# Optimization experiments

Hardware: AMD Instinct MI355X
Metric: run time of the kernel (lower is better)

## Reference

```python
import jax, jax.numpy as jnp
import numpy as np

N_NODES = 50000
N_EDGES = 800000
OBS_DIM = 25
HID = 128
EMB = 64
EDGE_DIM = 8
HEADS = 4
N_LAYERS = 3
COMM_RANGE = 1500.0
LN_EPS = 1e-5


def layernorm(x, g, b):
    mu = jnp.mean(x, axis=-1, keepdims=True)
    var = jnp.mean((x - mu) ** 2, axis=-1, keepdims=True)
    return (x - mu) / jnp.sqrt(var + LN_EPS) * g + b


def setup_inputs() -> dict:
    key = jax.random.key(0)
    ks = iter(jax.random.split(key, 64))

    def w(shape, s=0.05):
        return (jax.random.normal(next(ks), shape, jnp.float32) * s).astype(jnp.float32)

    inp = {}
    inp["observations"] = jax.random.normal(next(ks), (N_NODES, OBS_DIM), jnp.float32)
    inp["positions"] = jax.random.uniform(next(ks), (N_NODES, 2), jnp.float32) * 1000.0
    inp["edge_index"] = jax.random.randint(next(ks), (2, N_EDGES), 0, N_NODES, jnp.int32)
    # node encoder (obs_encoder branch: Linear-LN-ReLU-Linear-ReLU)
    inp["enc_w1"] = w((OBS_DIM, HID)); inp["enc_b1"] = w((HID,), 0.01)
    inp["enc_ln_g"] = jnp.ones((HID,), jnp.float32); inp["enc_ln_b"] = jnp.zeros((HID,), jnp.float32)
    inp["enc_w2"] = w((HID, EMB)); inp["enc_b2"] = w((EMB,), 0.01)
    cat_dim = 2 * EMB + EDGE_DIM  # 136
    # per-layer GNN params, stacked over layers
    inp["msg_w1"] = w((N_LAYERS, cat_dim, HID)); inp["msg_b1"] = w((N_LAYERS, HID), 0.01)
    inp["msg_w2"] = w((N_LAYERS, HID, EMB)); inp["msg_b2"] = w((N_LAYERS, EMB), 0.01)
    inp["att_w1"] = w((N_LAYERS, cat_dim, HID)); inp["att_b1"] = w((N_LAYERS, HID), 0.01)
    inp["att_w2"] = w((N_LAYERS, HID, HEADS)); inp["att_b2"] = w((N_LAYERS, HEADS), 0.01)
    inp["upd_w1"] = w((N_LAYERS, 2 * EMB, HID)); inp["upd_b1"] = w((N_LAYERS, HID), 0.01)
    inp["upd_w2"] = w((N_LAYERS, HID, EMB)); inp["upd_b2"] = w((N_LAYERS, EMB), 0.01)
    inp["ln_g"] = jnp.ones((N_LAYERS, EMB), jnp.float32); inp["ln_b"] = jnp.zeros((N_LAYERS, EMB), jnp.float32)
    # output projection
    inp["out_w1"] = w((EMB, HID)); inp["out_b1"] = w((HID,), 0.01)
    inp["out_w2"] = w((HID, EMB)); inp["out_b2"] = w((EMB,), 0.01)
    return inp


def reference(observations, positions, edge_index,
              enc_w1, enc_b1, enc_ln_g, enc_ln_b, enc_w2, enc_b2,
              msg_w1, msg_b1, msg_w2, msg_b2,
              att_w1, att_b1, att_w2, att_b2,
              upd_w1, upd_b1, upd_w2, upd_b2,
              ln_g, ln_b,
              out_w1, out_b1, out_w2, out_b2):
    n = observations.shape[0]
    # --- node encoder (use_full_obs=True path) ---
    h = observations @ enc_w1 + enc_b1
    h = jax.nn.relu(layernorm(h, enc_ln_g, enc_ln_b))
    x = jax.nn.relu(h @ enc_w2 + enc_b2)  # [N, EMB]

    # --- edge features (build_graph math, edges given) ---
    src, dst = edge_index[0], edge_index[1]
    rel = positions[dst] - positions[src]                    # [E, 2]
    dist = jnp.linalg.norm(rel, axis=-1, keepdims=True)      # [E, 1]
    rel_n = rel / (dist + 1e-6)
    dist_n = dist / COMM_RANGE
    angle = jnp.arctan2(rel[:, 1], rel[:, 0])[:, None]
    edge_attr = jnp.concatenate(
        [dist_n, rel_n, jnp.cos(angle), jnp.sin(angle), dist_n ** 2,
         jnp.zeros((rel.shape[0], 2), x.dtype)], axis=-1)    # [E, 8]

    # --- GNN communication layers (PyG: x_i = target = dst, x_j = source = src,
    #     aggregate to dst; dropout inactive at inference) ---
    for l in range(N_LAYERS):
        cat = jnp.concatenate([x[dst], x[src], edge_attr], axis=-1)       # [E, 136]
        m = jax.nn.relu(cat @ msg_w1[l] + msg_b1[l]) @ msg_w2[l] + msg_b2[l]   # [E, EMB]
        a = jax.nn.relu(cat @ att_w1[l] + att_b1[l]) @ att_w2[l] + att_b2[l]   # [E, HEADS]
        wgt = jnp.mean(jax.nn.softmax(a, axis=-1), axis=-1, keepdims=True)     # [E, 1]
        aggr = jax.ops.segment_sum(m * wgt, dst, num_segments=n)               # [N, EMB]
        upd_in = jnp.concatenate([x, aggr], axis=-1)                            # [N, 2*EMB]
        upd = jax.nn.relu(upd_in @ upd_w1[l] + upd_b1[l]) @ upd_w2[l] + upd_b2[l]
        x = layernorm(x + upd, ln_g[l], ln_b[l])

    # --- output projection ---
    return jax.nn.relu(x @ out_w1 + out_b1) @ out_w2 + out_b2
```

## Files before the change

### kernel.cpp

```cpp
#include <hip/hip_runtime.h>
#include <hip/hip_bf16.h>

typedef unsigned short ushort_t;
typedef unsigned int uint_t;

constexpr int OBS  = 25;
constexpr int HID  = 128;
constexpr int EMB  = 64;
constexpr int CAT  = 136;
constexpr int NN   = 50000;

constexpr int TE      = 128;
constexpr int ETHR    = 256;
constexpr int K1PAD   = 148;
constexpr int K2PAD   = 140;
constexpr int K1STEPS = 9;
constexpr int K2STEPS = 8;

constexpr int TB = 128;

typedef __attribute__((ext_vector_type(8)))  short bf16x8;
typedef __attribute__((ext_vector_type(16))) float f32x16;

__device__ __forceinline__ ushort_t f2bf(float f) {
    union { float f; uint_t u; } v; v.f = f;
    uint_t r = v.u + 0x7FFFu + ((v.u >> 16) & 1u);
    return (ushort_t)(r >> 16);
}

__device__ __forceinline__ bf16x8 ld8(const ushort_t* p) {
    uint2 lo = *reinterpret_cast<const uint2*>(p);
    uint2 hi = *reinterpret_cast<const uint2*>(p + 4);
    uint4 u = make_uint4(lo.x, lo.y, hi.x, hi.y);
    return __builtin_bit_cast(bf16x8, u);
}

#define CROW(R, LHI) (4 * (LHI) + ((R) & 3) + 8 * ((R) >> 2))

__global__ __launch_bounds__(256) void k_hist(
    const int* __restrict__ dst, int* __restrict__ hist, int ne)
{
    int e = blockIdx.x * 256 + threadIdx.x;
    if (e < ne) atomicAdd(&hist[dst[e]], 1);
}

__global__ __launch_bounds__(512) void k_scan1(
    const int* __restrict__ hist, int* __restrict__ scanned,
    int* __restrict__ bsum, int nn)
{
    __shared__ int s[512];
    int t = threadIdx.x, i = blockIdx.x * 512 + t;
    int v = (i < nn) ? hist[i] : 0;
    s[t] = v; __syncthreads();
#pragma unroll
    for (int off = 1; off < 512; off <<= 1) {
        int x = (t >= off) ? s[t - off] : 0;
        __syncthreads();
        s[t] += x;
        __syncthreads();
    }
    if (i < nn) scanned[i] = s[t] - v;
    if (t == 511) bsum[blockIdx.x] = s[511];
}

__global__ void k_scan2(int* __restrict__ bsum, int nb)
{
    if (blockIdx.x == 0 && threadIdx.x == 0) {
        int run = 0;
        for (int b = 0; b < nb; ++b) { int t = bsum[b]; bsum[b] = run; run += t; }
    }
}

__global__ __launch_bounds__(512) void k_scan3(
    int* __restrict__ scanned, const int* __restrict__ bsum, int nn)
{
    int i = blockIdx.x * 512 + threadIdx.x;
    if (i < nn) scanned[i] += bsum[blockIdx.x];
}

__global__ __launch_bounds__(256) void k_scatter_feat(
    const float* __restrict__ pos, const int* __restrict__ src,
    const int* __restrict__ dst, int* __restrict__ ofs,
    uint4* __restrict__ eab4, int* __restrict__ dsts, int ne)
{
    int e = blockIdx.x * 256 + threadIdx.x;
    if (e >= ne) return;
    int s = src[e], d = dst[e];
    float rx = pos[d * 2 + 0] - pos[s * 2 + 0];
    float ry = pos[d * 2 + 1] - pos[s * 2 + 1];
    float dist = sqrtf(rx * rx + ry * ry);
    float inv = 1.f / (dist + 1e-6f);
    float dn = dist * (1.f / 1500.f);
    float c, sn;
    if (dist > 0.f) { c = rx / dist; sn = ry / dist; } else { c = 1.f; sn = 0.f; }
    uint_t u0 = (uint_t)f2bf(dn)       | ((uint_t)f2bf(rx * inv) << 16);
    uint_t u1 = (uint_t)f2bf(ry * inv) | ((uint_t)f2bf(c) << 16);
    uint_t u2 = (uint_t)f2bf(sn)       | ((uint_t)f2bf(dn * dn) << 16);
    int p = atomicAdd(&ofs[d], 1);
    eab4[p] = make_uint4(u0, u1, u2, (uint_t)s);
    dsts[p] = d;
}

__global__ __launch_bounds__(256) void k_prep(
    const float* __restrict__ w1, const float* __restrict__ w2,
    ushort_t* __restrict__ w1t, ushort_t* __restrict__ w2t)
{
    int t = blockIdx.x * 256 + threadIdx.x;
    const int n1 = 3 * HID * K1PAD;
    if (t < n1) {
        int l = t / (HID * K1PAD), rem = t % (HID * K1PAD);
        int c = rem / K1PAD, k = rem % K1PAD;
        float v = (k < CAT) ? w1[(size_t)l * CAT * HID + (size_t)k * HID + c] : 0.f;
        w1t[t] = f2bf(v);
    }
    const int n2 = 3 * EMB * K2PAD;
    if (t < n2) {
        int l = t / (EMB * K2PAD), rem = t % (EMB * K2PAD);
        int c = rem / K2PAD, k = rem % K2PAD;
        float v = (k < HID) ? w2[(size_t)l * HID * EMB + (size_t)k * EMB + c] : 0.f;
        w2t[t] = f2bf(v);
    }
}

constexpr int EKP = 36;
__global__ __launch_bounds__(256, 1) void k_encoder_mfma(
    const float* __restrict__ obs,
    const float* __restrict__ w1, const float* __restrict__ b1,
    const float* __restrict__ lng, const float* __restrict__ lnb,
    const float* __restrict__ w2, const float* __restrict__ b2,
    float* __restrict__ x, ushort_t* __restrict__ xb, int n)
{
    __shared__ __align__(16) ushort_t s_OB[TB * EKP];
    __shared__ __align__(16) ushort_t s_B1[HID * EKP];
    __shared__ __align__(16) float    s_G[TB * 132];
    __shared__ __align__(16) ushort_t s_H[TB * K2PAD];
    __shared__ __align__(16) ushort_t s_W2[EMB * K2PAD];

    const int tid = threadIdx.x;
    const int lane = tid & 63, wid = tid >> 6;
    const int wr = wid >> 1, wc = wid & 1;
    const int l31 = lane & 31, lhi = lane >> 5;
    const int n0 = blockIdx.x * TB;

    for (int i = tid; i < TB * 32; i += 256) {
        int row = i >> 5, k = i & 31;
        int gn = n0 + row;
        float v = (gn < n && k < OBS) ? obs[(size_t)gn * OBS + k] : 0.f;
        s_OB[row * EKP + k] = f2bf(v);
    }
    for (int i = tid; i < 32 * HID; i += 256) {
        int k = i >> 7, c = i & 127;
        float v = (k < OBS) ? w1[k * HID + c] : 0.f;
        s_B1[c * EKP + k] = f2bf(v);
    }
    __syncthreads();

    f32x16 a00, a01, a10, a11;
    {
        float bv0 = b1[wc * 64 + l31], bv1 = b1[wc * 64 + 32 + l31];
#pragma unroll
        for (int i = 0; i < 16; ++i) { a00[i] = bv0; a01[i] = bv1; a10[i] = bv0; a11[i] = bv1; }
    }
    {
        const ushort_t* aR0 = s_OB + (wr * 64 + l31) * EKP;
        const ushort_t* aR1 = aR0 + 32 * EKP;
        const ushort_t* bR0 = s_B1 + (wc * 64 + l31) * EKP;
        const ushort_t* bR1 = bR0 + 32 * EKP;
        const int koff = lhi * 8;
#pragma unroll
        for (int s = 0; s < 2; ++s) {
            const int ke = s * 16 + koff;
            bf16x8 av0 = ld8(aR0 + ke), av1 = ld8(aR1 + ke);
            bf16x8 bv0 = ld8(bR0 + ke), bv1 = ld8(bR1 + ke);
            a00 = __builtin_amdgcn_mfma_f32_32x32x16_bf16(av0, bv0, a00, 0, 0, 0);
            a01 = __builtin_amdgcn_mfma_f32_32x32x16_bf16(av0, bv1, a01, 0, 0, 0);
            a10 = __builtin_amdgcn_mfma_f32_32x32x16_bf16(av1, bv0, a10, 0, 0, 0);
            a11 = __builtin_amdgcn_mfma_f32_32x32x16_bf16(av1, bv1, a11, 0, 0, 0);
        }
    }
#define WRITE_G(ACC, SUB, NC)                                                  \
    {                                                                          \
        const int col = wc * 64 + (NC) * 32 + l31;                             \
        _Pragma("unroll")                                                      \
        for (int r = 0; r < 16; ++r) {                                         \
            int row = wr * 64 + (SUB) * 32 + CROW(r, lhi);                     \
            s_G[row * 132 + col] = ACC[r];                                     \
        }                                                                      \
    }
    WRITE_G(a00, 0, 0) WRITE_G(a01, 0, 1) WRITE_G(a10, 1, 0) WRITE_G(a11, 1, 1)
#undef WRITE_G
    __syncthreads();

    for (int i = tid; i < HID * EMB; i += 256) {
        int k = i >> 6, c = i & 63;
        s_W2[c * K2PAD + k] = f2bf(w2[i]);
    }
    if (tid < TB) {
        float sum = 0.f, sum2 = 0.f;
        const float* gr = s_G + tid * 132;
#pragma unroll 8
        for (int q = 0; q < HID; ++q) { float v = gr[q]; sum += v; sum2 += v * v; }
        float mu = sum * (1.f / HID);
        float var = fmaxf(sum2 * (1.f / HID) - mu * mu, 0.f);
        float rs = 1.f / sqrtf(var + 1e-5f);
        ushort_t* hr = s_H + tid * K2PAD;
#pragma unroll 8
        for (int q = 0; q < HID; ++q) {
            float v = (gr[q] - mu) * rs * lng[q] + lnb[q];
            hr[q] = f2bf(fmaxf(v, 0.f));
        }
    }
    __syncthreads();

    f32x16 c0, c1;
    {
        float bv = b2[wc * 32 + l31];
#pragma unroll
        for (int i = 0; i < 16; ++i) { c0[i] = bv; c1[i] = bv; }
    }
    {
        const ushort_t* aR0 = s_H + (wr * 64 + l31) * K2PAD;
        const ushort_t* aR1 = aR0 + 32 * K2PAD;
        const ushort_t* bR = s_W2 + (wc * 32 + l31) * K2PAD;
        const int koff = lhi * 8;
#pragma unroll
        for (int s = 0; s < K2STEPS; ++s) {
            const int ke = s * 16 + koff;
            bf16x8 av0 = ld8(aR0 + ke), av1 = ld8(aR1 + ke);
            bf16x8 bv = ld8(bR + ke);
            c0 = __builtin_amdgcn_mfma_f32_32x32x16_bf16(av0, bv, c0, 0, 0, 0);
            c1 = __builtin_amdgcn_mfma_f32_32x32x16_bf16(av1, bv, c1, 0, 0, 0);
        }
    }
    {
        const int col = wc * 32 + l31;
#define STORE_X(CC, SUB)                                                       \
        {                                                                      \
            _Pragma("unroll")                                                  \
            for (int r = 0; r < 16; ++r) {                                     \
                int row = wr * 64 + (SUB) * 32 + CROW(r, lhi);                 \
                int gn = n0 + row;                                             \
                if (gn < n) {                                                  \
                    float v = fmaxf(CC[r], 0.f);                               \
                    x[(size_t)gn * EMB + col] = v;                             \
                    xb[(size_t)gn * EMB + col] = f2bf(v);                      \
                }                                                              \
            }                                                                  \
        }
        STORE_X(c0, 0) STORE_X(c1, 1)
#undef STORE_X
    }
}

__global__ __launch_bounds__(ETHR, 4) void k_edge_mfma(
    const ushort_t* __restrict__ xb,
    const uint4* __restrict__ eab4,
    const int* __restrict__ dsts,
    const ushort_t* __restrict__ w1t,
    const float* __restrict__ b1,
    const ushort_t* __restrict__ w2t,
    const float* __restrict__ b2,
    float* __restrict__ aggr, int ne)
{
    __shared__ __align__(16) ushort_t s_A[TE * K1PAD];
    __shared__ int s_dst[TE];
    ushort_t* s_H = s_A;
    float*    s_M = reinterpret_cast<float*>(s_A);

    const int tid  = threadIdx.x;
    const int lane = tid & 63, wid = tid >> 6;
    const int wr = wid >> 1, wc = wid & 1;
    const int l31 = lane & 31, lhi = lane >> 5;
    const int e0 = blockIdx.x * TE;

    if (tid < TE) s_dst[tid] = dsts[e0 + tid];
    {
        const int e = tid >> 1, h = tid & 1, ge = e0 + e;
        ushort_t* arow = s_A + e * K1PAD;
        if (h == 0) {
            int d = dsts[ge];
            const uint2* sp = reinterpret_cast<const uint2*>(xb + (size_t)d * EMB);
            uint2* dp = reinterpret_cast<uint2*>(arow);
#pragma unroll
            for (int i = 0; i < 16; ++i) dp[i] = sp[i];
        } else {
            uint4 ev = eab4[ge];
            int s = (int)ev.w;
            const uint2* sp = reinterpret_cast<const uint2*>(xb + (size_t)s * EMB);
            uint2* dp = reinterpret_cast<uint2*>(arow + EMB);
#pragma unroll
            for (int i = 0; i < 16; ++i) dp[i] = sp[i];
            uint2* ap = reinterpret_cast<uint2*>(arow + 2 * EMB);
            ap[0] = make_uint2(ev.x, ev.y);
            ap[1] = make_uint2(ev.z, 0u);
            uint2* pp = reinterpret_cast<uint2*>(arow + CAT);
            pp[0] = make_uint2(0u, 0u); pp[1] = make_uint2(0u, 0u); pp[2] = make_uint2(0u, 0u);
        }
    }
    __syncthreads();

    f32x16 a00, a01, a10, a11;
    {
        float bv0 = b1[wc * 64 + l31], bv1 = b1[wc * 64 + 32 + l31];
#pragma unroll
        for (int i = 0; i < 16; ++i) { a00[i] = bv0; a01[i] = bv1; a10[i] = bv0; a11[i] = bv1; }
    }
    {
        const ushort_t* aR0 = s_A + (wr * 64 + l31) * K1PAD;
        const ushort_t* aR1 = aR0 + 32 * K1PAD;
        const ushort_t* bR0 = w1t + (wc * 64 + l31) * K1PAD;
        const ushort_t* bR1 = bR0 + 32 * K1PAD;
        const int koff = lhi * 8;
#pragma unroll
        for (int s = 0; s < K1STEPS; ++s) {
            const int ke = s * 16 + koff;
            bf16x8 av0 = ld8(aR0 + ke);
            bf16x8 av1 = ld8(aR1 + ke);
            bf16x8 bv0 = ld8(bR0 + ke);
            bf16x8 bv1 = ld8(bR1 + ke);
            a00 = __builtin_amdgcn_mfma_f32_32x32x16_bf16(av0, bv0, a00, 0, 0, 0);
            a01 = __builtin_amdgcn_mfma_f32_32x32x16_bf16(av0, bv1, a01, 0, 0, 0);
            a10 = __builtin_amdgcn_mfma_f32_32x32x16_bf16(av1, bv0, a10, 0, 0, 0);
            a11 = __builtin_amdgcn_mfma_f32_32x32x16_bf16(av1, bv1, a11, 0, 0, 0);
        }
    }
    __syncthreads();

#define WRITE_H(ACC, SUB, NC)                                                  \
    {                                                                          \
        const int col = wc * 64 + (NC) * 32 + l31;                             \
        _Pragma("unroll")                                                      \
        for (int r = 0; r < 16; ++r) {                                         \
            int row = wr * 64 + (SUB) * 32 + CROW(r, lhi);                     \
            s_H[row * K2PAD + col] = f2bf(fmaxf(ACC[r], 0.f));                 \
        }                                                                      \
    }
    WRITE_H(a00, 0, 0) WRITE_H(a01, 0, 1) WRITE_H(a10, 1, 0) WRITE_H(a11, 1, 1)
#undef WRITE_H
    __syncthreads();

    f32x16 c0, c1;
    {
        float bv = b2[wc * 32 + l31];
#pragma unroll
        for (int i = 0; i < 16; ++i) { c0[i] = bv; c1[i] = bv; }
    }
    {
        const ushort_t* aR0 = s_H + (wr * 64 + l31) * K2PAD;
        const ushort_t* aR1 = aR0 + 32 * K2PAD;
        const ushort_t* bR = w2t + (wc * 32 + l31) * K2PAD;
        const int koff = lhi * 8;
#pragma unroll
        for (int s = 0; s < K2STEPS; ++s) {
            const int ke = s * 16 + koff;
            bf16x8 av0 = ld8(aR0 + ke);
            bf16x8 av1 = ld8(aR1 + ke);
            bf16x8 bv = ld8(bR + ke);
            c0 = __builtin_amdgcn_mfma_f32_32x32x16_bf16(av0, bv, c0, 0, 0, 0);
            c1 = __builtin_amdgcn_mfma_f32_32x32x16_bf16(av1, bv, c1, 0, 0, 0);
        }
    }
    __syncthreads();

    {
        const int col = wc * 32 + l31;
#pragma unroll
        for (int r = 0; r < 16; ++r) {
            int row = wr * 64 + CROW(r, lhi);
            s_M[row * 68 + col] = c0[r] * 0.25f;
            s_M[(row + 32) * 68 + col] = c1[r] * 0.25f;
        }
    }
    __syncthreads();

    {
        const int col = tid & 63, g = tid >> 6, base = g * 32;
        int cur = s_dst[base];
        float acc = 0.f;
#pragma unroll 8
        for (int r = 0; r < 32; ++r) {
            int d = s_dst[base + r];
            float v = s_M[(base + r) * 68 + col];
            if (d != cur) {
                atomicAdd(aggr + (size_t)cur * EMB + col, acc);
                acc = 0.f; cur = d;
            }
            acc += v;
        }
        atomicAdd(aggr + (size_t)cur * EMB + col, acc);
    }
}

__global__ __launch_bounds__(256, 2) void k_update_mfma(
    float* __restrict__ x, ushort_t* __restrict__ xb,
    const float* __restrict__ aggr,
    const float* __restrict__ w1, const float* __restrict__ b1,
    const float* __restrict__ w2, const float* __restrict__ b2,
    const float* __restrict__ g, const float* __restrict__ bb, int n)
{
    __shared__ __align__(16) ushort_t s_A[TB * K2PAD];
    __shared__ __align__(16) ushort_t s_B[TB * K2PAD];
    ushort_t* s_H  = s_A;
    ushort_t* s_W2 = s_B;
    float*    s_U  = reinterpret_cast<float*>(s_B);

    const int tid = threadIdx.x;
    const int lane = tid & 63, wid = tid >> 6;
    const int wr = wid >> 1, wc = wid & 1;
    const int l31 = lane & 31, lhi = lane >> 5;
    const int n0 = blockIdx.x * TB;

    {
        const int row = tid >> 1, h = tid & 1;
        const int gn = n0 + row;
        ushort_t* arow = s_A + row * K2PAD;
        if (h == 0) {
            uint2* dp = reinterpret_cast<uint2*>(arow);
            if (gn < n) {
                const uint2* sp = reinterpret_cast<const uint2*>(xb + (size_t)gn * EMB);
#pragma unroll
                for (int i = 0; i < 16; ++i) dp[i] = sp[i];
            } else {
                const uint2 z = make_uint2(0u, 0u);
#pragma unroll
                for (int i = 0; i < 16; ++i) dp[i] = z;
            }
        } else {
            if (gn < n) {
                const float4* sp = reinterpret_cast<const float4*>(aggr + (size_t)gn * EMB);
#pragma unroll
                for (int i = 0; i < 16; ++i) {
                    float4 v = sp[i];
                    ushort_t* q = arow + EMB + i * 4;
                    q[0] = f2bf(v.x); q[1] = f2bf(v.y); q[2] = f2bf(v.z); q[3] = f2bf(v.w);
                }
            } else {
#pragma unroll
                for (int i = 0; i < 16; ++i) {
                    ushort_t* q = arow + EMB + i * 4;
                    q[0] = 0; q[1] = 0; q[2] = 0; q[3] = 0;
                }
            }
        }
    }
    for (int i = tid; i < 128 * 128; i += 256) {
        int k = i >> 7, c = i & 127;
        s_B[c * K2PAD + k] = f2bf(w1[i]);
    }
    __syncthreads();

    f32x16 a00, a01, a10, a11;
    {
        float bv0 = b1[wc * 64 + l31], bv1 = b1[wc * 64 + 32 + l31];
#pragma unroll
        for (int i = 0; i < 16; ++i) { a00[i] = bv0; a01[i] = bv1; a10[i] = bv0; a11[i] = bv1; }
    }
    {
        const ushort_t* aR0 = s_A + (wr * 64 + l31) * K2PAD;
        const ushort_t* aR1 = aR0 + 32 * K2PAD;
        const ushort_t* bR0 = s_B + (wc * 64 + l31) * K2PAD;
        const ushort_t* bR1 = bR0 + 32 * K2PAD;
        const int koff = lhi * 8;
#pragma unroll
        for (int s = 0; s < K2STEPS; ++s) {
            const int ke = s * 16 + koff;
            bf16x8 av0 = ld8(aR0 + ke), av1 = ld8(aR1 + ke);
            bf16x8 bv0 = ld8(bR0 + ke), bv1 = ld8(bR1 + ke);
            a00 = __builtin_amdgcn_mfma_f32_32x32x16_bf16(av0, bv0, a00, 0, 0, 0);
            a01 = __builtin_amdgcn_mfma_f32_32x32x16_bf16(av0, bv1, a01, 0, 0, 0);
            a10 = __builtin_amdgcn_mfma_f32_32x32x16_bf16(av1, bv0, a10, 0, 0, 0);
            a11 = __builtin_amdgcn_mfma_f32_32x32x16_bf16(av1, bv1, a11, 0, 0, 0);
        }
    }
    __syncthreads();

#define WRITE_H(ACC, SUB, NC)                                                  \
    {                                                                          \
        const int col = wc * 64 + (NC) * 32 + l31;                             \
        _Pragma("unroll")                                                      \
        for (int r = 0; r < 16; ++r) {                                         \
            int row = wr * 64 + (SUB) * 32 + CROW(r, lhi);                     \
            s_H[row * K2PAD + col] = f2bf(fmaxf(ACC[r], 0.f));                 \
        }                                                                      \
    }
    WRITE_H(a00, 0, 0) WRITE_H(a01, 0, 1) WRITE_H(a10, 1, 0) WRITE_H(a11, 1, 1)
#undef WRITE_H
    for (int i = tid; i < HID * EMB; i += 256) {
        int k = i >> 6, c = i & 63;
        s_W2[c * K2PAD + k] = f2bf(w2[i]);
    }
    __syncthreads();

    f32x16 c0, c1;
    {
        float bv = b2[wc * 32 + l31];
#pragma unroll
        for (int i = 0; i < 16; ++i) { c0[i] = bv; c1[i] = bv; }
    }
    {
        const ushort_t* aR0 = s_H + (wr * 64 + l31) * K2PAD;
        const ushort_t* aR1 = aR0 + 32 * K2PAD;
        const ushort_t* bR = s_W2 + (wc * 32 + l31) * K2PAD;
        const int koff = lhi * 8;
#pragma unroll
        for (int s = 0; s < K2STEPS; ++s) {
            const int ke = s * 16 + koff;
            bf16x8 av0 = ld8(aR0 + ke), av1 = ld8(aR1 + ke);
            bf16x8 bv = ld8(bR + ke);
            c0 = __builtin_amdgcn_mfma_f32_32x32x16_bf16(av0, bv, c0, 0, 0, 0);
            c1 = __builtin_amdgcn_mfma_f32_32x32x16_bf16(av1, bv, c1, 0, 0, 0);
        }
    }
    __syncthreads();

    {
        const int col = wc * 32 + l31;
#pragma unroll
        for (int r = 0; r < 16; ++r) {
            int row = wr * 64 + CROW(r, lhi);
            s_U[row * 68 + col] = c0[r];
            s_U[(row + 32) * 68 + col] = c1[r];
        }
    }
    __syncthreads();

    if (tid < TB) {
        int gn = n0 + tid;
        if (gn < n) {
            const float* xr = x + (size_t)gn * EMB;
            float* ur = s_U + tid * 68;
            float sum = 0.f, sum2 = 0.f;
#pragma unroll 8
            for (int q = 0; q < EMB; ++q) {
                float v = xr[q] + ur[q];
                ur[q] = v;
                sum += v; sum2 += v * v;
            }
            float mu = sum * (1.f / EMB);
            float var = fmaxf(sum2 * (1.f / EMB) - mu * mu, 0.f);
            float rs = 1.f / sqrtf(var + 1e-5f);
            float* xo = x + (size_t)gn * EMB;
            ushort_t* xbo = xb + (size_t)gn * EMB;
#pragma unroll 8
            for (int q = 0; q < EMB; ++q) {
                float v = (ur[q] - mu) * rs * g[q] + bb[q];
                xo[q] = v;
                xbo[q] = f2bf(v);
            }
        }
    }
}

constexpr int OKP = 68;
__global__ __launch_bounds__(256, 2) void k_output_mfma(
    const ushort_t* __restrict__ xb,
    const float* __restrict__ w1, const float* __restrict__ b1,
    const float* __restrict__ w2, const float* __restrict__ b2,
    float* __restrict__ out, int n)
{
    __shared__ __align__(16) ushort_t s_A[TB * OKP];
    __shared__ __align__(16) ushort_t s_B[HID * OKP];
    __shared__ __align__(16) ushort_t s_H[TB * K2PAD];
    __shared__ __align__(16) ushort_t s_W2[EMB * K2PAD];

    const int tid = threadIdx.x;
    const int lane = tid & 63, wid = tid >> 6;
    const int wr = wid >> 1, wc = wid & 1;
    const int l31 = lane & 31, lhi = lane >> 5;
    const int n0 = blockIdx.x * TB;

    for (int i = tid; i < TB * 16; i += 256) {
        int row = i >> 4, q = i & 15;
        int gn = n0 + row;
        uint2 v = make_uint2(0u, 0u);
        if (gn < n) v = reinterpret_cast<const uint2*>(xb + (size_t)gn * EMB)[q];
        *reinterpret_cast<uint2*>(s_A + row * OKP + q * 4) = v;
    }
    for (int i = tid; i < EMB * HID; i += 256) {
        int k = i >> 7, c = i & 127;
        s_B[c * OKP + k] = f2bf(w1[i]);
    }
    for (int i = tid; i < HID * EMB; i += 256) {
        int k = i >> 6, c = i & 63;
        s_W2[c * K2PAD + k] = f2bf(w2[i]);
    }
    __syncthreads();

    f32x16 a00, a01, a10, a11;
    {
        float bv0 = b1[wc * 64 + l31], bv1 = b1[wc * 64 + 32 + l31];
#pragma unroll
        for (int i = 0; i < 16; ++i) { a00[i] = bv0; a01[i] = bv1; a10[i] = bv0; a11[i] = bv1; }
    }
    {
        const ushort_t* aR0 = s_A + (wr * 64 + l31) * OKP;
        const ushort_t* aR1 = aR0 + 32 * OKP;
        const ushort_t* bR0 = s_B + (wc * 64 + l31) * OKP;
        const ushort_t* bR1 = bR0 + 32 * OKP;
        const int koff = lhi * 8;
#pragma unroll
        for (int s = 0; s < 4; ++s) {
            const int ke = s * 16 + koff;
            bf16x8 av0 = ld8(aR0 + ke), av1 = ld8(aR1 + ke);
            bf16x8 bv0 = ld8(bR0 + ke), bv1 = ld8(bR1 + ke);
            a00 = __builtin_amdgcn_mfma_f32_32x32x16_bf16(av0, bv0, a00, 0, 0, 0);
            a01 = __builtin_amdgcn_mfma_f32_32x32x16_bf16(av0, bv1, a01, 0, 0, 0);
            a10 = __builtin_amdgcn_mfma_f32_32x32x16_bf16(av1, bv0, a10, 0, 0, 0);
            a11 = __builtin_amdgcn_mfma_f32_32x32x16_bf16(av1, bv1, a11, 0, 0, 0);
        }
    }
    __syncthreads();

#define WRITE_H(ACC, SUB, NC)                                                  \
    {                                                                          \
        const int col = wc * 64 + (NC) * 32 + l31;                             \
        _Pragma("unroll")                                                      \
        for (int r = 0; r < 16; ++r) {                                         \
            int row = wr * 64 + (SUB) * 32 + CROW(r, lhi);                     \
            s_H[row * K2PAD + col] = f2bf(fmaxf(ACC[r], 0.f));                 \
        }                                                                      \
    }
    WRITE_H(a00, 0, 0) WRITE_H(a01, 0, 1) WRITE_H(a10, 1, 0) WRITE_H(a11, 1, 1)
#undef WRITE_H
    __syncthreads();

    f32x16 c0, c1;
    {
        float bv = b2[wc * 32 + l31];
#pragma unroll
        for (int i = 0; i < 16; ++i) { c0[i] = bv; c1[i] = bv; }
    }
    {
        const ushort_t* aR0 = s_H + (wr * 64 + l31) * K2PAD;
        const ushort_t* aR1 = aR0 + 32 * K2PAD;
        const ushort_t* bR = s_W2 + (wc * 32 + l31) * K2PAD;
        const int koff = lhi * 8;
#pragma unroll
        for (int s = 0; s < K2STEPS; ++s) {
            const int ke = s * 16 + koff;
            bf16x8 av0 = ld8(aR0 + ke), av1 = ld8(aR1 + ke);
            bf16x8 bv = ld8(bR + ke);
            c0 = __builtin_amdgcn_mfma_f32_32x32x16_bf16(av0, bv, c0, 0, 0, 0);
            c1 = __builtin_amdgcn_mfma_f32_32x32x16_bf16(av1, bv, c1, 0, 0, 0);
        }
    }
    {
        const int col = wc * 32 + l31;
#pragma unroll
        for (int r = 0; r < 16; ++r) {
            int row0 = wr * 64 + CROW(r, lhi);
            int g0 = n0 + row0, g1 = g0 + 32;
            if (g0 < n) out[(size_t)g0 * EMB + col] = c0[r];
            if (g1 < n) out[(size_t)g1 * EMB + col] = c1[r];
        }
    }
}

extern "C" void kernel_launch(void* const* d_in, const int* in_sizes, int n_in,
                              void* d_out, int out_size, void* d_ws, size_t ws_size,
                              hipStream_t stream)
{
    const float* obs     = (const float*)d_in[0];
    const float* pos     = (const float*)d_in[1];
    const int*   eidx    = (const int*)d_in[2];
    const float* enc_w1  = (const float*)d_in[3];
    const float* enc_b1  = (const float*)d_in[4];
    const float* enc_lng = (const float*)d_in[5];
    const float* enc_lnb = (const float*)d_in[6];
    const float* enc_w2  = (const float*)d_in[7];
    const float* enc_b2  = (const float*)d_in[8];
    const float* msg_w1  = (const float*)d_in[9];
    const float* msg_b1  = (const float*)d_in[10];
    const float* msg_w2  = (const float*)d_in[11];
    const float* msg_b2  = (const float*)d_in[12];
    const float* upd_w1  = (const float*)d_in[17];
    const float* upd_b1  = (const float*)d_in[18];
    const float* upd_w2  = (const float*)d_in[19];
    const float* upd_b2  = (const float*)d_in[20];
    const float* ln_g    = (const float*)d_in[21];
    const float* ln_b    = (const float*)d_in[22];
    const float* out_w1  = (const float*)d_in[23];
    const float* out_b1  = (const float*)d_in[24];
    const float* out_w2  = (const float*)d_in[25];
    const float* out_b2  = (const float*)d_in[26];

    const int n  = in_sizes[0] / OBS;
    const int ne = in_sizes[2] / 2;
    const int* src = eidx;
    const int* dst = eidx + ne;

    char* ws = (char*)d_ws;
    float*    x     = (float*)ws;
    ushort_t* xbuf  = (ushort_t*)(ws + 12800000);
    uint4*    eab4  = (uint4*)(ws + 19200000);
    float*    aggr  = (float*)(ws + 32000000);
    ushort_t* w1t   = (ushort_t*)(ws + 44800000);
    ushort_t* w2t   = (ushort_t*)(ws + 44913664);
    int*      dsts  = (int*)(ws + 44967424);
    int*      hist  = (int*)(ws + 48167424);
    int*      scan  = (int*)(ws + 48367424);
    int*      bsum  = (int*)(ws + 48567424);

    const int NB1 = (NN + 511) / 512;
    const int nb  = (n + TB - 1) / TB;

    hipMemsetAsync(hist, 0, NN * sizeof(int), stream);
    k_hist<<<(ne + 255) / 256, 256, 0, stream>>>(dst, hist, ne);
    k_scan1<<<NB1, 512, 0, stream>>>(hist, scan, bsum, NN);
    k_scan2<<<1, 64, 0, stream>>>(bsum, NB1);
    k_scan3<<<NB1, 512, 0, stream>>>(scan, bsum, NN);
    k_scatter_feat<<<(ne + 255) / 256, 256, 0, stream>>>(pos, src, dst, scan,
                                                         eab4, dsts, ne);

    k_prep<<<(3 * HID * K1PAD + 255) / 256, 256, 0, stream>>>(msg_w1, msg_w2, w1t, w2t);
    k_encoder_mfma<<<nb, 256, 0, stream>>>(obs, enc_w1, enc_b1, enc_lng, enc_lnb,
                                           enc_w2, enc_b2, x, xbuf, n);

    for (int l = 0; l < 3; ++l) {
        hipMemsetAsync(aggr, 0, (size_t)n * EMB * sizeof(float), stream);
        k_edge_mfma<<<ne / TE, ETHR, 0, stream>>>(
            xbuf, eab4, dsts,
            w1t + (size_t)l * HID * K1PAD, msg_b1 + (size_t)l * HID,
            w2t + (size_t)l * EMB * K2PAD, msg_b2 + (size_t)l * EMB,
            aggr, ne);
        k_update_mfma<<<nb, 256, 0, stream>>>(
            x, xbuf, aggr,
            upd_w1 + (size_t)l * 2 * EMB * HID, upd_b1 + (size_t)l * HID,
            upd_w2 + (size_t)l * HID * EMB, upd_b2 + (size_t)l * EMB,
            ln_g + (size_t)l * EMB, ln_b + (size_t)l * EMB, n);
    }
    k_output_mfma<<<nb, 256, 0, stream>>>(
        xbuf, out_w1, out_b1, out_w2, out_b2, (float*)d_out, n);
}
```

Measured before the change: 771.6 us.

## Pack dst into edge records, enlarge edge tiles, swizzle blocks, store interior runs

Edge features are now packed into a compact record that carries both src and dst. This removes the separate dsts array, and the cos, sin and squared-distance features are rebuilt inside the edge kernel. The edge kernel tile grows to 256 edges with 512 threads and a wider K padding, and gathers use 16-byte loads. Blocks are remapped so that contiguous edge ranges stay on the same XCD, and segment runs that lie entirely inside a tile are written with plain stores instead of atomics. The cost targeted is edge-kernel memory traffic and atomic contention. The risks are register pressure from the 512x4 launch bounds, higher LDS use per block, and a longer serial reduction over 64 rows per thread.

```diff
diff --git a/kernel.cpp b/kernel.cpp
--- a/kernel.cpp
+++ b/kernel.cpp
@@ -10,9 +10,9 @@
 constexpr int CAT  = 136;
 constexpr int NN   = 50000;
 
-constexpr int TE      = 128;
-constexpr int ETHR    = 256;
-constexpr int K1PAD   = 148;
+constexpr int TE      = 256;
+constexpr int ETHR    = 512;
+constexpr int K1PAD   = 152;
 constexpr int K2PAD   = 140;
 constexpr int K1STEPS = 9;
 constexpr int K2STEPS = 8;
@@ -81,7 +81,7 @@
 __global__ __launch_bounds__(256) void k_scatter_feat(
     const float* __restrict__ pos, const int* __restrict__ src,
     const int* __restrict__ dst, int* __restrict__ ofs,
-    uint4* __restrict__ eab4, int* __restrict__ dsts, int ne)
+    uint4* __restrict__ eab4, int ne)
 {
     int e = blockIdx.x * 256 + threadIdx.x;
     if (e >= ne) return;
@@ -91,14 +91,10 @@
     float dist = sqrtf(rx * rx + ry * ry);
     float inv = 1.f / (dist + 1e-6f);
     float dn = dist * (1.f / 1500.f);
-    float c, sn;
-    if (dist > 0.f) { c = rx / dist; sn = ry / dist; } else { c = 1.f; sn = 0.f; }
-    uint_t u0 = (uint_t)f2bf(dn)       | ((uint_t)f2bf(rx * inv) << 16);
-    uint_t u1 = (uint_t)f2bf(ry * inv) | ((uint_t)f2bf(c) << 16);
-    uint_t u2 = (uint_t)f2bf(sn)       | ((uint_t)f2bf(dn * dn) << 16);
+    uint_t ux = (uint_t)f2bf(dn) | ((uint_t)f2bf(rx * inv) << 16);
+    uint_t uy = (uint_t)f2bf(ry * inv) | ((dist > 0.f ? 0u : 1u) << 16);
     int p = atomicAdd(&ofs[d], 1);
-    eab4[p] = make_uint4(u0, u1, u2, (uint_t)s);
-    dsts[p] = d;
+    eab4[p] = make_uint4(ux, uy, (uint_t)s, (uint_t)d);
 }
 
 __global__ __launch_bounds__(256) void k_prep(
@@ -255,7 +251,6 @@
 __global__ __launch_bounds__(ETHR, 4) void k_edge_mfma(
     const ushort_t* __restrict__ xb,
     const uint4* __restrict__ eab4,
-    const int* __restrict__ dsts,
     const ushort_t* __restrict__ w1t,
     const float* __restrict__ b1,
     const ushort_t* __restrict__ w2t,
@@ -271,30 +266,41 @@
     const int lane = tid & 63, wid = tid >> 6;
     const int wr = wid >> 1, wc = wid & 1;
     const int l31 = lane & 31, lhi = lane >> 5;
-    const int e0 = blockIdx.x * TE;
-
-    if (tid < TE) s_dst[tid] = dsts[e0 + tid];
+
+    const int nwg = ne / TE;
+    const int q = nwg >> 3, rr = nwg & 7;
+    const int bid = blockIdx.x;
+    const int xcd = bid & 7, loc = bid >> 3;
+    const int swz = (xcd < rr ? xcd * (q + 1) : rr * (q + 1) + (xcd - rr) * q) + loc;
+    const int e0 = swz * TE;
+
     {
         const int e = tid >> 1, h = tid & 1, ge = e0 + e;
         ushort_t* arow = s_A + e * K1PAD;
+        uint4 ev = eab4[ge];
         if (h == 0) {
-            int d = dsts[ge];
-            const uint2* sp = reinterpret_cast<const uint2*>(xb + (size_t)d * EMB);
-            uint2* dp = reinterpret_cast<uint2*>(arow);
-#pragma unroll
-            for (int i = 0; i < 16; ++i) dp[i] = sp[i];
+            s_dst[e] = (int)ev.w;
+            const uint4* sp = reinterpret_cast<const uint4*>(xb + (size_t)ev.w * EMB);
+            uint4* dp = reinterpret_cast<uint4*>(arow);
+#pragma unroll
+            for (int i = 0; i < 8; ++i) dp[i] = sp[i];
         } else {
-            uint4 ev = eab4[ge];
-            int s = (int)ev.w;
-            const uint2* sp = reinterpret_cast<const uint2*>(xb + (size_t)s * EMB);
-            uint2* dp = reinterpret_cast<uint2*>(arow + EMB);
-#pragma unroll
-            for (int i = 0; i < 16; ++i) dp[i] = sp[i];
-            uint2* ap = reinterpret_cast<uint2*>(arow + 2 * EMB);
-            ap[0] = make_uint2(ev.x, ev.y);
-            ap[1] = make_uint2(ev.z, 0u);
-            uint2* pp = reinterpret_cast<uint2*>(arow + CAT);
-            pp[0] = make_uint2(0u, 0u); pp[1] = make_uint2(0u, 0u); pp[2] = make_uint2(0u, 0u);
+            const uint4* sp = reinterpret_cast<const uint4*>(xb + (size_t)ev.z * EMB);
+            uint4* dp = reinterpret_cast<uint4*>(arow + EMB);
+#pragma unroll
+            for (int i = 0; i < 8; ++i) dp[i] = sp[i];
+            uint_t dn_b = ev.x & 0xFFFFu, rxn_b = ev.x >> 16;
+            uint_t ryn_b = ev.y & 0xFFFFu, flag = ev.y >> 16;
+            uint_t cos_b = flag ? 0x3F80u : rxn_b;
+            uint_t sin_b = flag ? 0u : ryn_b;
+            union { uint_t u; float f; } cv; cv.u = dn_b << 16;
+            uint_t dn2_b = (uint_t)f2bf(cv.f * cv.f);
+            uint4* fp4 = reinterpret_cast<uint4*>(arow + 2 * EMB);
+            fp4[0] = make_uint4(dn_b | (rxn_b << 16), ryn_b | (cos_b << 16),
+                                sin_b | (dn2_b << 16), 0u);
+            uint4* pp = reinterpret_cast<uint4*>(arow + CAT);
+            pp[0] = make_uint4(0u, 0u, 0u, 0u);
+            pp[1] = make_uint4(0u, 0u, 0u, 0u);
         }
     }
     __syncthreads();
@@ -373,17 +379,20 @@
     }
     __syncthreads();
 
-    {
-        const int col = tid & 63, g = tid >> 6, base = g * 32;
+    if (tid < 256) {
+        const int col = tid & 63, grp = tid >> 6, base = grp * 64;
         int cur = s_dst[base];
+        int runstart = 0;
         float acc = 0.f;
-#pragma unroll 8
-        for (int r = 0; r < 32; ++r) {
+#pragma unroll 4
+        for (int r = 0; r < 64; ++r) {
             int d = s_dst[base + r];
             float v = s_M[(base + r) * 68 + col];
             if (d != cur) {
-                atomicAdd(aggr + (size_t)cur * EMB + col, acc);
-                acc = 0.f; cur = d;
+                float* p = aggr + (size_t)cur * EMB + col;
+                if (runstart == 0) atomicAdd(p, acc);
+                else *p = acc;
+                acc = 0.f; cur = d; runstart = r;
             }
             acc += v;
         }
@@ -431,14 +440,14 @@
 #pragma unroll
                 for (int i = 0; i < 16; ++i) {
                     float4 v = sp[i];
-                    ushort_t* q = arow + EMB + i * 4;
-                    q[0] = f2bf(v.x); q[1] = f2bf(v.y); q[2] = f2bf(v.z); q[3] = f2bf(v.w);
+                    ushort_t* qq = arow + EMB + i * 4;
+                    qq[0] = f2bf(v.x); qq[1] = f2bf(v.y); qq[2] = f2bf(v.z); qq[3] = f2bf(v.w);
                 }
             } else {
 #pragma unroll
                 for (int i = 0; i < 16; ++i) {
-                    ushort_t* q = arow + EMB + i * 4;
-                    q[0] = 0; q[1] = 0; q[2] = 0; q[3] = 0;
+                    ushort_t* qq = arow + EMB + i * 4;
+                    qq[0] = 0; qq[1] = 0; qq[2] = 0; qq[3] = 0;
                 }
             }
         }
@@ -695,11 +704,10 @@
     uint4*    eab4  = (uint4*)(ws + 19200000);
     float*    aggr  = (float*)(ws + 32000000);
     ushort_t* w1t   = (ushort_t*)(ws + 44800000);
-    ushort_t* w2t   = (ushort_t*)(ws + 44913664);
-    int*      dsts  = (int*)(ws + 44967424);
-    int*      hist  = (int*)(ws + 48167424);
-    int*      scan  = (int*)(ws + 48367424);
-    int*      bsum  = (int*)(ws + 48567424);
+    ushort_t* w2t   = (ushort_t*)(ws + 44916736);
+    int*      hist  = (int*)(ws + 44970496);
+    int*      scan  = (int*)(ws + 45170496);
+    int*      bsum  = (int*)(ws + 45370496);
 
     const int NB1 = (NN + 511) / 512;
     const int nb  = (n + TB - 1) / TB;
@@ -710,7 +718,7 @@
     k_scan2<<<1, 64, 0, stream>>>(bsum, NB1);
     k_scan3<<<NB1, 512, 0, stream>>>(scan, bsum, NN);
     k_scatter_feat<<<(ne + 255) / 256, 256, 0, stream>>>(pos, src, dst, scan,
-                                                         eab4, dsts, ne);
+                                                         eab4, ne);
 
     k_prep<<<(3 * HID * K1PAD + 255) / 256, 256, 0, stream>>>(msg_w1, msg_w2, w1t, w2t);
     k_encoder_mfma<<<nb, 256, 0, stream>>>(obs, enc_w1, enc_b1, enc_lng, enc_lnb,
@@ -719,7 +727,7 @@
     for (int l = 0; l < 3; ++l) {
         hipMemsetAsync(aggr, 0, (size_t)n * EMB * sizeof(float), stream);
         k_edge_mfma<<<ne / TE, ETHR, 0, stream>>>(
-            xbuf, eab4, dsts,
+            xbuf, eab4,
             w1t + (size_t)l * HID * K1PAD, msg_b1 + (size_t)l * HID,
             w2t + (size_t)l * EMB * K2PAD, msg_b2 + (size_t)l * EMB,
             aggr, ne);
```

Result: slower. 820.7 us (+6.4%).
